# Kernel optimization log

Measured on AMD Instinct MI355X. Metric: run time of the kernel, lower is better.

## Reference

```python
import jax, jax.numpy as jnp
import numpy as np

B, V, CIN, H, W = 2, 4, 256, 96, 96
COUT, VS = 32, 64


def setup_inputs() -> dict:
    key = jax.random.key(0)
    k1, k2, k3, k4, k5 = jax.random.split(key, 5)
    features = jax.random.normal(k1, (B, V, CIN, H, W), dtype=jnp.float32)
    proj_matricies = jax.random.normal(k2, (B, V, 3, 4), dtype=jnp.float32)
    coord_volumes = jax.random.normal(k3, (B, VS, VS, VS, 3), dtype=jnp.float32) * 1000.0
    W_proc = jax.random.normal(k4, (COUT, CIN), dtype=jnp.float32) * 0.05
    b_proc = jax.random.normal(k5, (COUT,), dtype=jnp.float32) * 0.01
    return {"features": features, "proj_matricies": proj_matricies,
            "coord_volumes": coord_volumes, "W_proc": W_proc, "b_proc": b_proc}


def _bilinear_sample(feat, x, y):
    # feat: [C, H, W]; x, y: [N] pixel coords (align_corners=True mapping already applied)
    Hh, Ww = feat.shape[1], feat.shape[2]
    x0 = jnp.floor(x).astype(jnp.int32); x1 = x0 + 1
    y0 = jnp.floor(y).astype(jnp.int32); y1 = y0 + 1
    wx1 = x - x0; wx0 = 1.0 - wx1
    wy1 = y - y0; wy0 = 1.0 - wy1

    def gather(xi, yi):
        valid = ((xi >= 0) & (xi < Ww) & (yi >= 0) & (yi < Hh)).astype(feat.dtype)
        xc = jnp.clip(xi, 0, Ww - 1); yc = jnp.clip(yi, 0, Hh - 1)
        return feat[:, yc, xc] * valid  # [C, N] (zeros padding)

    return (gather(x0, y0) * (wx0 * wy0)
            + gather(x1, y0) * (wx1 * wy0)
            + gather(x0, y1) * (wx0 * wy1)
            + gather(x1, y1) * (wx1 * wy1))


def reference(features, proj_matricies, coord_volumes, W_proc, b_proc):
    b, v, cin, h, w = features.shape
    vs = coord_volumes.shape[1]
    # 1x1 conv (process_feature)
    feats = jnp.einsum('bvchw,oc->bvohw', features, W_proc) + b_proc[None, None, :, None, None]
    c = feats.shape[2]
    # homogeneous 3D grid points: [B, N, 4]
    pts = coord_volumes.reshape(b, -1, 3)
    pts_h = jnp.concatenate([pts, jnp.ones(pts.shape[:-1] + (1,), pts.dtype)], axis=-1)
    # project to image plane: [B, V, N, 3] homogeneous (u, v, w)
    proj_pts = jnp.einsum('bvij,bnj->bvni', proj_matricies, pts_h)
    wz = proj_pts[..., 2]
    invalid = wz <= 0.0
    wz_safe = jnp.where(wz == 0.0, 1.0, wz)
    u = proj_pts[..., 0] / wz_safe
    ve = proj_pts[..., 1] / wz_safe
    # normalized grid coords (faithful to original: x divided by feature_shape[0]=H, y by feature_shape[1]=W)
    gx = 2.0 * (u / h - 0.5)
    gy = 2.0 * (ve / w - 0.5)
    # align_corners=True pixel coords: x indexes width, y indexes height
    px = (gx + 1.0) * 0.5 * (w - 1)
    py = (gy + 1.0) * 0.5 * (h - 1)
    # sample per (batch, view): [B, V, C, N]
    sampled = jax.vmap(jax.vmap(_bilinear_sample))(feats, px, py)
    sampled = jnp.where(invalid[:, :, None, :], 0.0, sampled)
    # softmax over views per (b, c, voxel), weighted sum
    weights = jax.nn.softmax(sampled, axis=1)
    vol = jnp.sum(sampled * weights, axis=1)  # [B, C, N]
    return vol.reshape(b, c, vs, vs, vs)
```

## Files before the change

### kernel.cpp

```cpp
#include <hip/hip_runtime.h>
#include <hip/hip_bf16.h>

#define CIN   256
#define COUT  32
#define IMG_H 96
#define IMG_W 96
#define HW    (IMG_H*IMG_W)
#define NB    2
#define NV    4
#define VSZ   64
#define NVOX  (VSZ*VSZ*VSZ)

__global__ __launch_bounds__(256) void conv1x1_kernel(
    const float* __restrict__ features,
    const float* __restrict__ Wp,
    const float* __restrict__ bp,
    __hip_bfloat16* __restrict__ out)
{
    __shared__ float Wt[CIN*COUT];
    __shared__ float Pp[4*64*36];
    const int tid = threadIdx.x;
    #pragma unroll
    for (int i = 0; i < CIN*COUT/256; ++i) {
        int idx = i*256 + tid;
        Wt[idx] = Wp[(idx & 31)*CIN + (idx >> 5)];
    }
    __syncthreads();

    const int w    = tid >> 6;
    const int lane = tid & 63;
    const int bv   = blockIdx.y;
    const int px0  = blockIdx.x*64;
    const float* f = features + (size_t)bv*CIN*HW + (size_t)(w*64)*HW + px0 + lane;

    float acc[32];
    #pragma unroll
    for (int o = 0; o < 32; ++o) acc[o] = (w == 0) ? bp[o] : 0.f;

    const float* wrow = &Wt[(w*64)*COUT];
    for (int cc = 0; cc < 64; cc += 16) {
        float x[16];
        #pragma unroll
        for (int i = 0; i < 16; ++i)
            x[i] = f[(size_t)(cc + i)*HW];
        #pragma unroll
        for (int i = 0; i < 16; ++i) {
            const float4* wr = (const float4*)(wrow + (size_t)(cc + i)*COUT);
            const float4 w0 = wr[0], w1 = wr[1], w2 = wr[2], w3 = wr[3];
            const float xi = x[i];
            acc[ 0] += xi*w0.x; acc[ 1] += xi*w0.y; acc[ 2] += xi*w0.z; acc[ 3] += xi*w0.w;
            acc[ 4] += xi*w1.x; acc[ 5] += xi*w1.y; acc[ 6] += xi*w1.z; acc[ 7] += xi*w1.w;
            acc[ 8] += xi*w2.x; acc[ 9] += xi*w2.y; acc[10] += xi*w2.z; acc[11] += xi*w2.w;
            acc[12] += xi*w3.x; acc[13] += xi*w3.y; acc[14] += xi*w3.z; acc[15] += xi*w3.w;
            const float4* wr2 = wr + 4;
            const float4 w4 = wr2[0], w5 = wr2[1], w6 = wr2[2], w7 = wr2[3];
            acc[16] += xi*w4.x; acc[17] += xi*w4.y; acc[18] += xi*w4.z; acc[19] += xi*w4.w;
            acc[20] += xi*w5.x; acc[21] += xi*w5.y; acc[22] += xi*w5.z; acc[23] += xi*w5.w;
            acc[24] += xi*w6.x; acc[25] += xi*w6.y; acc[26] += xi*w6.z; acc[27] += xi*w6.w;
            acc[28] += xi*w7.x; acc[29] += xi*w7.y; acc[30] += xi*w7.z; acc[31] += xi*w7.w;
        }
    }

    #pragma unroll
    for (int j = 0; j < 8; ++j)
        *(float4*)(&Pp[(w*64 + lane)*36 + j*4]) =
            make_float4(acc[4*j], acc[4*j+1], acc[4*j+2], acc[4*j+3]);
    __syncthreads();

    const int px = tid >> 2, cg = tid & 3;
    float r[8];
    #pragma unroll
    for (int j = 0; j < 8; ++j) r[j] = 0.f;
    #pragma unroll
    for (int ww = 0; ww < 4; ++ww) {
        const float4* p = (const float4*)(&Pp[(ww*64 + px)*36 + cg*8]);
        const float4 a = p[0], b2 = p[1];
        r[0] += a.x;  r[1] += a.y;  r[2] += a.z;  r[3] += a.w;
        r[4] += b2.x; r[5] += b2.y; r[6] += b2.z; r[7] += b2.w;
    }
    union { uint4 u4; __hip_bfloat16 h[8]; } pk;
    #pragma unroll
    for (int j = 0; j < 8; ++j) pk.h[j] = __float2bfloat16(r[j]);
    *(uint4*)(out + ((size_t)(bv*HW + px0 + px))*COUT + cg*8) = pk.u4;
}

__global__ __launch_bounds__(256) void volgen_kernel(
    const __hip_bfloat16* __restrict__ feats,
    const float* __restrict__ proj,
    const float* __restrict__ coords,
    float* __restrict__ out)
{
    __shared__ float T[COUT*65];
    const int tid = threadIdx.x;
    const int vl  = tid >> 2;
    const int cg  = tid & 3;
    const int b   = blockIdx.y;
    const int n   = blockIdx.x*64 + vl;

    const float* cp = coords + ((size_t)b*NVOX + n)*3;
    const float X = cp[0], Y = cp[1], Z = cp[2];

    int   off[NV][4];
    float wgt[NV][4];
    #pragma unroll
    for (int v = 0; v < NV; ++v) {
        const float* P = proj + (size_t)(b*NV + v)*12;
        const float wz = P[8]*X + P[9]*Y + P[10]*Z + P[11];
        const bool  vz = wz > 0.f;
        const float rz = __builtin_amdgcn_rcpf(wz);
        float px = (P[0]*X + P[1]*Y + P[2]*Z + P[3]) * rz * (95.f/96.f);
        float py = (P[4]*X + P[5]*Y + P[6]*Z + P[7]) * rz * (95.f/96.f);
        px = vz ? px : 0.f;  py = vz ? py : 0.f;
        px = fminf(fmaxf(px, -1.0e6f), 1.0e6f);
        py = fminf(fmaxf(py, -1.0e6f), 1.0e6f);
        const float fx0 = floorf(px), fy0 = floorf(py);
        const int x0 = (int)fx0, y0 = (int)fy0, x1 = x0+1, y1 = y0+1;
        const float wx1 = px - fx0, wx0 = 1.f - wx1;
        const float wy1 = py - fy0, wy0 = 1.f - wy1;
        const bool vx0 = (unsigned)x0 < (unsigned)IMG_W;
        const bool vx1 = (unsigned)x1 < (unsigned)IMG_W;
        const bool vy0 = (unsigned)y0 < (unsigned)IMG_H;
        const bool vy1 = (unsigned)y1 < (unsigned)IMG_H;
        const int cx0 = min(max(x0, 0), IMG_W-1), cx1 = min(max(x1, 0), IMG_W-1);
        const int cy0 = min(max(y0, 0), IMG_H-1), cy1 = min(max(y1, 0), IMG_H-1);
        const int base = ((b*NV + v)*HW)*COUT + cg*8;
        off[v][0] = base + (cy0*IMG_W + cx0)*COUT;  wgt[v][0] = (vz & vx0 & vy0) ? wx0*wy0 : 0.f;
        off[v][1] = base + (cy0*IMG_W + cx1)*COUT;  wgt[v][1] = (vz & vx1 & vy0) ? wx1*wy0 : 0.f;
        off[v][2] = base + (cy1*IMG_W + cx0)*COUT;  wgt[v][2] = (vz & vx0 & vy1) ? wx0*wy1 : 0.f;
        off[v][3] = base + (cy1*IMG_W + cx1)*COUT;  wgt[v][3] = (vz & vx1 & vy1) ? wx1*wy1 : 0.f;
    }

    uint4 t[NV][4];
    #pragma unroll
    for (int v = 0; v < NV; ++v)
        #pragma unroll
        for (int c = 0; c < 4; ++c)
            t[v][c] = *(const uint4*)(feats + off[v][c]);

    float A[8], Bs[8];
    #pragma unroll
    for (int j = 0; j < 8; ++j) { A[j] = 0.f; Bs[j] = 0.f; }

    #pragma unroll
    for (int v = 0; v < NV; ++v) {
        float s[8];
        #pragma unroll
        for (int j = 0; j < 8; ++j) s[j] = 0.f;
        #pragma unroll
        for (int c = 0; c < 4; ++c) {
            const float w = wgt[v][c];
            const unsigned tu[4] = { t[v][c].x, t[v][c].y, t[v][c].z, t[v][c].w };
            #pragma unroll
            for (int k = 0; k < 4; ++k) {
                s[2*k]   += w * __uint_as_float(tu[k] << 16);
                s[2*k+1] += w * __uint_as_float(tu[k] & 0xffff0000u);
            }
        }
        #pragma unroll
        for (int j = 0; j < 8; ++j) {
            const float e = __expf(s[j]);
            A[j] += e;  Bs[j] += s[j]*e;
        }
    }

    #pragma unroll
    for (int j = 0; j < 8; ++j)
        T[(cg*8 + j)*65 + vl] = Bs[j] * __builtin_amdgcn_rcpf(A[j]);
    __syncthreads();

    const size_t ob = (size_t)b*COUT*NVOX + (size_t)blockIdx.x*64;
    #pragma unroll
    for (int i = 0; i < 8; ++i) {
        const int idx = i*256 + tid;
        const int ch = idx >> 6, vx = idx & 63;
        out[ob + (size_t)ch*NVOX + vx] = T[ch*65 + vx];
    }
}

extern "C" void kernel_launch(void* const* d_in, const int* in_sizes, int n_in,
                              void* d_out, int out_size, void* d_ws, size_t ws_size,
                              hipStream_t stream)
{
    const float* features = (const float*)d_in[0];
    const float* proj     = (const float*)d_in[1];
    const float* coords   = (const float*)d_in[2];
    const float* Wp       = (const float*)d_in[3];
    const float* bp       = (const float*)d_in[4];
    float* out = (float*)d_out;
    __hip_bfloat16* featsT = (__hip_bfloat16*)d_ws;

    hipLaunchKernelGGL(conv1x1_kernel, dim3(HW/64, NB*NV), dim3(256), 0, stream,
                       features, Wp, bp, featsT);
    hipLaunchKernelGGL(volgen_kernel, dim3(NVOX/64, NB), dim3(256), 0, stream,
                       featsT, proj, coords, out);
}
```

Before: 222.0 us.

## Split conv1x1 across output-channel groups and read weights as uniform scalars

Each wave now computes 8 output channels over all 256 input channels for its 64 pixels, in place of splitting the input channels across waves. This drops the shared-memory weight transpose, the cross-wave partial-sum reduction and both barriers. Weights are read through a wave-uniform pointer so they can be fetched as scalar loads. The cost is that each feature value is now read by all four waves of a block, quadrupling global feature loads, which may only be absorbed if the caches catch the repeats.

```diff
diff --git a/kernel.cpp b/kernel.cpp
--- a/kernel.cpp
+++ b/kernel.cpp
@@ -17,71 +17,34 @@
     const float* __restrict__ bp,
     __hip_bfloat16* __restrict__ out)
 {
-    __shared__ float Wt[CIN*COUT];
-    __shared__ float Pp[4*64*36];
-    const int tid = threadIdx.x;
+    const int og   = __builtin_amdgcn_readfirstlane((threadIdx.x >> 6) & 3);
+    const int lane = threadIdx.x & 63;
+    const int bv   = blockIdx.y;
+    const int px   = blockIdx.x*64 + lane;
+    const float* f     = features + (size_t)bv*CIN*HW + px;
+    const float* wbase = Wp + (size_t)og*8*CIN;
+
+    float acc[8];
     #pragma unroll
-    for (int i = 0; i < CIN*COUT/256; ++i) {
-        int idx = i*256 + tid;
-        Wt[idx] = Wp[(idx & 31)*CIN + (idx >> 5)];
-    }
-    __syncthreads();
+    for (int j = 0; j < 8; ++j) acc[j] = bp[og*8 + j];
 
-    const int w    = tid >> 6;
-    const int lane = tid & 63;
-    const int bv   = blockIdx.y;
-    const int px0  = blockIdx.x*64;
-    const float* f = features + (size_t)bv*CIN*HW + (size_t)(w*64)*HW + px0 + lane;
-
-    float acc[32];
-    #pragma unroll
-    for (int o = 0; o < 32; ++o) acc[o] = (w == 0) ? bp[o] : 0.f;
-
-    const float* wrow = &Wt[(w*64)*COUT];
-    for (int cc = 0; cc < 64; cc += 16) {
-        float x[16];
+    for (int cc = 0; cc < CIN; cc += 8) {
+        float x[8];
         #pragma unroll
-        for (int i = 0; i < 16; ++i)
+        for (int i = 0; i < 8; ++i)
             x[i] = f[(size_t)(cc + i)*HW];
         #pragma unroll
-        for (int i = 0; i < 16; ++i) {
-            const float4* wr = (const float4*)(wrow + (size_t)(cc + i)*COUT);
-            const float4 w0 = wr[0], w1 = wr[1], w2 = wr[2], w3 = wr[3];
-            const float xi = x[i];
-            acc[ 0] += xi*w0.x; acc[ 1] += xi*w0.y; acc[ 2] += xi*w0.z; acc[ 3] += xi*w0.w;
-            acc[ 4] += xi*w1.x; acc[ 5] += xi*w1.y; acc[ 6] += xi*w1.z; acc[ 7] += xi*w1.w;
-            acc[ 8] += xi*w2.x; acc[ 9] += xi*w2.y; acc[10] += xi*w2.z; acc[11] += xi*w2.w;
-            acc[12] += xi*w3.x; acc[13] += xi*w3.y; acc[14] += xi*w3.z; acc[15] += xi*w3.w;
-            const float4* wr2 = wr + 4;
-            const float4 w4 = wr2[0], w5 = wr2[1], w6 = wr2[2], w7 = wr2[3];
-            acc[16] += xi*w4.x; acc[17] += xi*w4.y; acc[18] += xi*w4.z; acc[19] += xi*w4.w;
-            acc[20] += xi*w5.x; acc[21] += xi*w5.y; acc[22] += xi*w5.z; acc[23] += xi*w5.w;
-            acc[24] += xi*w6.x; acc[25] += xi*w6.y; acc[26] += xi*w6.z; acc[27] += xi*w6.w;
-            acc[28] += xi*w7.x; acc[29] += xi*w7.y; acc[30] += xi*w7.z; acc[31] += xi*w7.w;
+        for (int i = 0; i < 8; ++i) {
+            #pragma unroll
+            for (int j = 0; j < 8; ++j)
+                acc[j] += x[i] * wbase[(size_t)j*CIN + cc + i];
         }
     }
 
-    #pragma unroll
-    for (int j = 0; j < 8; ++j)
-        *(float4*)(&Pp[(w*64 + lane)*36 + j*4]) =
-            make_float4(acc[4*j], acc[4*j+1], acc[4*j+2], acc[4*j+3]);
-    __syncthreads();
-
-    const int px = tid >> 2, cg = tid & 3;
-    float r[8];
-    #pragma unroll
-    for (int j = 0; j < 8; ++j) r[j] = 0.f;
-    #pragma unroll
-    for (int ww = 0; ww < 4; ++ww) {
-        const float4* p = (const float4*)(&Pp[(ww*64 + px)*36 + cg*8]);
-        const float4 a = p[0], b2 = p[1];
-        r[0] += a.x;  r[1] += a.y;  r[2] += a.z;  r[3] += a.w;
-        r[4] += b2.x; r[5] += b2.y; r[6] += b2.z; r[7] += b2.w;
-    }
     union { uint4 u4; __hip_bfloat16 h[8]; } pk;
     #pragma unroll
-    for (int j = 0; j < 8; ++j) pk.h[j] = __float2bfloat16(r[j]);
-    *(uint4*)(out + ((size_t)(bv*HW + px0 + px))*COUT + cg*8) = pk.u4;
+    for (int j = 0; j < 8; ++j) pk.h[j] = __float2bfloat16(acc[j]);
+    *(uint4*)(out + ((size_t)(bv*HW + px))*COUT + og*8) = pk.u4;
 }
 
 __global__ __launch_bounds__(256) void volgen_kernel(
```

Result: faster. 188.9 us (-14.9%).
